# Performance work log

Hardware: AMD Instinct MI355X
Metric: run time of the kernel (lower is better)

Reference implementation:

```python
import jax, jax.numpy as jnp
import numpy as np

# ---- config constants (cfg) ----
AA, LP, Tc = 1.0, 1.0, 1.0
OMEGA_PHI, ALPHA_PHI, Lc = 1.0, 0.01, 1.0
CSE, CLE = 0.5, 0.00574
AC_PRE_SCALE = 1.0
AC1 = 2 * AA * LP * Tc
AC2 = LP * OMEGA_PHI * Tc
AC3 = LP * ALPHA_PHI * Tc / Lc**2

N, HID, NLAYERS, EMB = 65536, 128, 4, 64  # 2*EMB == HID


def setup_inputs() -> dict:
    key = jax.random.key(0)
    ks = jax.random.split(key, 6)
    x = jax.random.uniform(ks[0], (N, 2), dtype=jnp.float32)
    t = jax.random.uniform(ks[1], (N, 1), dtype=jnp.float32)
    B = jax.random.normal(ks[2], (3, EMB), dtype=jnp.float32)  # fourier features
    Wh = jax.random.normal(ks[3], (NLAYERS, HID, HID), dtype=jnp.float32) / np.sqrt(HID)
    bh = jnp.zeros((NLAYERS, HID), dtype=jnp.float32)
    Wout = jax.random.normal(ks[4], (HID, 2), dtype=jnp.float32) / np.sqrt(HID)
    bout = jnp.zeros((2,), dtype=jnp.float32)
    return {"x": x, "t": t, "B": B, "Wh": Wh, "bh": bh, "Wout": Wout, "bout": bout}


def reference(x, t, B, Wh, bh, Wout, bout):
    mirror = jnp.array([-1.0, 1.0], dtype=x.dtype)

    def mlp(xx, tt):  # xx:(2,), tt:(1,) -> (2,)
        z = jnp.concatenate([xx, tt])              # (3,)
        f = 2 * jnp.pi * (z @ B)                   # (EMB,)
        h = jnp.concatenate([jnp.sin(f), jnp.cos(f)])  # (HID,)
        def layer(h, wb):
            W, b = wb
            return jnp.tanh(h @ W + b), None
        h, _ = jax.lax.scan(layer, h, (Wh, bh))
        return h @ Wout + bout

    def net_u(xx, tt):  # hard-constrained (phi, c), symmetrized in x
        def hard_cons(xx_):
            phi, cl = jnp.tanh(mlp(xx_, tt)) / 2 + 0.5
            cl = cl * (1 - CSE + CLE)
            c = (CSE - CLE) * (-2 * phi**3 + 3 * phi**2) + cl
            return jnp.stack([phi, c])
        return (hard_cons(xx) + hard_cons(xx * mirror)) / 2

    def net_ac_point(xx, tt):  # Allen-Cahn residual at one collocation point
        phi, c = net_u(xx, tt)
        h_phi = -2 * phi**3 + 3 * phi**2
        dh_dphi = -6 * phi**2 + 6 * phi
        dg_dphi = 4 * phi**3 - 6 * phi**2 + 2 * phi
        dphi_dt = jax.jacrev(lambda t_: net_u(xx, t_)[0])(tt)          # (1,)
        hess = jax.hessian(lambda x_: net_u(x_, tt)[0])(xx)            # (2,2)
        nabla2phi = jnp.trace(hess)
        ac = (dphi_dt.squeeze()
              - AC1 * (c - h_phi * (CSE - CLE) - CLE) * (CSE - CLE) * dh_dphi
              + AC2 * dg_dphi
              - AC3 * nabla2phi)
        return ac / AC_PRE_SCALE

    return jax.vmap(net_ac_point)(x, t)  # (N,) PDE residuals
```

## Files before the change

kernel.cpp:

```cpp
#include <hip/hip_runtime.h>
#include <math.h>

#define NPTS_PER_WAVE 6

typedef _Float16 h8 __attribute__((ext_vector_type(8)));
typedef _Float16 h2 __attribute__((ext_vector_type(2)));
typedef __fp16   fp16x2 __attribute__((ext_vector_type(2)));
typedef float    f4 __attribute__((ext_vector_type(4)));
typedef unsigned int uint32;

#define CSE_C 0.5f
#define CLE_C 0.00574f
#define DCOEF (CSE_C - CLE_C)
#define KCOEF (1.0f - CSE_C + CLE_C)

__device__ __forceinline__ float tanh_fast(float xx) {
    float e = __expf(2.0f * xx);
    float r = __builtin_amdgcn_rcpf(e + 1.0f);
    return fmaf(-2.0f, r, 1.0f);
}
__device__ __forceinline__ unsigned short f2h(float a) {
    union { _Float16 h; unsigned short u; } ua; ua.h = (_Float16)a; return ua.u;
}
__device__ __forceinline__ h2 pkrtz(float a, float b) {
    union { fp16x2 f; h2 h; } x; x.f = __builtin_amdgcn_cvt_pkrtz(a, b); return x.h;
}
__device__ __forceinline__ uint32 pk2h(float a, float b) {
    union { h2 h; uint32 u; } x; x.h = pkrtz(a, b); return x.u;
}
__device__ __forceinline__ h8 h8_from4(uint32 a, uint32 b, uint32 c, uint32 d) {
    union { uint32 u[4]; h8 v; } x; x.u[0] = a; x.u[1] = b; x.u[2] = c; x.u[3] = d;
    return x.v;
}

extern "C" __global__ __launch_bounds__(256)
void pinn_prep(const float* __restrict__ Wh, uint32* __restrict__ Wp)
{
    int gid  = blockIdx.x * 256 + threadIdx.x;
    int d    = gid & 3;
    int lane = (gid >> 2) & 63;
    int kt   = (gid >> 8) & 3;
    int jo   = (gid >> 10) & 7;
    int L    = gid >> 13;
    int j    = kt * 32 + (lane >> 4) * 8 + 2 * d;
    int jout = jo * 16 + (lane & 15);
    float w0 = Wh[(L * 128 + j) * 128 + jout];
    float w1 = Wh[(L * 128 + j + 1) * 128 + jout];
    Wp[gid] = pk2h(w0, w1);
}

extern "C" __global__ __launch_bounds__(64, 2)
void pinn_mfma(const float* __restrict__ x, const float* __restrict__ t,
               const float* __restrict__ B, const uint32* __restrict__ Wp,
               const float* __restrict__ bh, const float* __restrict__ Wout,
               const float* __restrict__ bout, float* __restrict__ out, int npts)
{
    __shared__ __align__(16) unsigned short H[64][136];

    const int lane = threadIdx.x;
    const int c    = lane & 15;
    const int g    = lane >> 4;
    const int base_pt = blockIdx.x * NPTS_PER_WAVE;

    unsigned short* Hb = &H[0][0];

    uint4 wt[2][4];
    {
        const uint4* W0 = (const uint4*)Wp;
        #pragma unroll
        for (int kt = 0; kt < 4; ++kt) wt[0][kt] = W0[kt * 64 + lane];
        #pragma unroll
        for (int kt = 0; kt < 4; ++kt) wt[1][kt] = W0[(4 + kt) * 64 + lane];
    }

    {
        const float TWO_PI = 6.28318530717958647692f;
        const float Br0 = B[lane], Br1 = B[64 + lane], Br2 = B[128 + lane];
        const float b0 = TWO_PI * Br0, b1 = TWO_PI * Br1, b2 = TWO_PI * Br2;
        const float bsq = fmaf(b0, b0, b1 * b1);
        #pragma unroll
        for (int pl = 0; pl < 6; ++pl) {
            int pt = base_pt + pl; if (pt > npts - 1) pt = npts - 1;
            const float2 xx = *(const float2*)&x[2 * pt];
            const float tt = t[pt];
            const float uc = fmaf(xx.y, Br1, tt * Br2);
            const float ux = xx.x * Br0;
            #pragma unroll
            for (int mir = 0; mir < 2; ++mir) {
                float u = mir ? (uc - ux) : (uc + ux);
                float r = u - floorf(u);
                float sf = __builtin_amdgcn_sinf(r);
                float cf = __builtin_amdgcn_cosf(r);
                const int b  = pl * 2 + mir;
                const int rs = (b / 3) * 16 + (b % 3) * 5;
                Hb[(rs + 0) * 136 + lane] = f2h(sf);
                Hb[(rs + 1) * 136 + lane] = f2h(cf * b2);
                Hb[(rs + 2) * 136 + lane] = f2h(cf * b0);
                Hb[(rs + 3) * 136 + lane] = f2h(cf * b1);
                Hb[(rs + 4) * 136 + lane] = f2h(-sf * bsq);
                Hb[(rs + 0) * 136 + 64 + lane] = f2h(cf);
                Hb[(rs + 1) * 136 + 64 + lane] = f2h(-sf * b2);
                Hb[(rs + 2) * 136 + 64 + lane] = f2h(-sf * b0);
                Hb[(rs + 3) * 136 + 64 + lane] = f2h(-sf * b1);
                Hb[(rs + 4) * 136 + 64 + lane] = f2h(-cf * bsq);
            }
        }
    }
    asm volatile("s_waitcnt lgkmcnt(0)" ::: "memory");

    for (int L = 0; L < 4; ++L) {
        h8 bf[4][4];
        #pragma unroll
        for (int ct = 0; ct < 4; ++ct)
            #pragma unroll
            for (int kt = 0; kt < 4; ++kt)
                bf[ct][kt] = *(const h8*)&Hb[(ct * 16 + c) * 136 + kt * 32 + g * 8];

        const uint4* WL = (const uint4*)Wp + (size_t)L * 2048;
        const uint4* WN = WL + 2048;

        #pragma unroll
        for (int jo = 0; jo < 8; ++jo) {
            const int cur = jo & 1;
            f4 a0 = {0.f, 0.f, 0.f, 0.f}, a1 = {0.f, 0.f, 0.f, 0.f};
            f4 a2 = {0.f, 0.f, 0.f, 0.f}, a3 = {0.f, 0.f, 0.f, 0.f};
            #pragma unroll
            for (int kt = 0; kt < 4; ++kt) {
                union { uint4 u; h8 v; } af;
                af.u = wt[cur][kt];
                a0 = __builtin_amdgcn_mfma_f32_16x16x32_f16(af.v, bf[0][kt], a0, 0, 0, 0);
                a1 = __builtin_amdgcn_mfma_f32_16x16x32_f16(af.v, bf[1][kt], a1, 0, 0, 0);
                a2 = __builtin_amdgcn_mfma_f32_16x16x32_f16(af.v, bf[2][kt], a2, 0, 0, 0);
                a3 = __builtin_amdgcn_mfma_f32_16x16x32_f16(af.v, bf[3][kt], a3, 0, 0, 0);
            }
            if (jo < 6) {
                #pragma unroll
                for (int kt = 0; kt < 4; ++kt)
                    wt[cur][kt] = WL[((jo + 2) * 4 + kt) * 64 + lane];
            } else if (L < 3) {
                #pragma unroll
                for (int kt = 0; kt < 4; ++kt)
                    wt[cur][kt] = WN[((jo - 6) * 4 + kt) * 64 + lane];
            }
            union { h2 h[2]; uint2 u; } w0, w1, w2, w3;
            w0.h[0] = pkrtz(a0[0], a0[1]); w0.h[1] = pkrtz(a0[2], a0[3]);
            w1.h[0] = pkrtz(a1[0], a1[1]); w1.h[1] = pkrtz(a1[2], a1[3]);
            w2.h[0] = pkrtz(a2[0], a2[1]); w2.h[1] = pkrtz(a2[2], a2[3]);
            w3.h[0] = pkrtz(a3[0], a3[1]); w3.h[1] = pkrtz(a3[2], a3[3]);
            *(uint2*)&Hb[(0  + c) * 136 + jo * 16 + g * 4] = w0.u;
            *(uint2*)&Hb[(16 + c) * 136 + jo * 16 + g * 4] = w1.u;
            *(uint2*)&Hb[(32 + c) * 136 + jo * 16 + g * 4] = w2.u;
            *(uint2*)&Hb[(48 + c) * 136 + jo * 16 + g * 4] = w3.u;
        }
        asm volatile("s_waitcnt lgkmcnt(0)" ::: "memory");

        {
            const int jb = 2 * lane;
            const float2 bj = *(const float2*)&bh[L * 128 + jb];
            const h2 bias2 = pkrtz(bj.x, bj.y);
            const h2 m2 = {(_Float16)(-2.0f), (_Float16)(-2.0f)};
            #pragma unroll
            for (int b = 0; b < 12; ++b) {
                const int rs = (b / 3) * 16 + (b % 3) * 5;
                h2 vp = *(const h2*)&Hb[(rs + 0) * 136 + jb];
                h2 tp = *(const h2*)&Hb[(rs + 1) * 136 + jb];
                h2 pp = *(const h2*)&Hb[(rs + 2) * 136 + jb];
                h2 qp = *(const h2*)&Hb[(rs + 3) * 136 + jb];
                h2 Lp = *(const h2*)&Hb[(rs + 4) * 136 + jb];
                vp = vp + bias2;
                float y0 = tanh_fast((float)vp[0]);
                float y1 = tanh_fast((float)vp[1]);
                h2 yp = pkrtz(y0, y1);
                h2 sp = pkrtz(fmaf(-y0, y0, 1.f), fmaf(-y1, y1, 1.f));
                h2 qq = __builtin_elementwise_fma(pp, pp, qp * qp);
                h2 Ln = sp * __builtin_elementwise_fma(yp * m2, qq, Lp);
                *(h2*)&Hb[(rs + 0) * 136 + jb] = yp;
                *(h2*)&Hb[(rs + 1) * 136 + jb] = sp * tp;
                *(h2*)&Hb[(rs + 2) * 136 + jb] = sp * pp;
                *(h2*)&Hb[(rs + 3) * 136 + jb] = sp * qp;
                *(h2*)&Hb[(rs + 4) * 136 + jb] = Ln;
            }
        }
        asm volatile("s_waitcnt lgkmcnt(0)" ::: "memory");
    }

    {
        h8 afo[4];
        const int   mc  = c & 1;
        const float sel = (c < 2) ? 1.0f : 0.0f;
        #pragma unroll
        for (int kt = 0; kt < 4; ++kt) {
            uint32 u[4];
            #pragma unroll
            for (int d = 0; d < 4; ++d) {
                int k = kt * 32 + g * 8 + 2 * d;
                float w0 = Wout[k * 2 + mc] * sel;
                float w1 = Wout[(k + 1) * 2 + mc] * sel;
                u[d] = pk2h(w0, w1);
            }
            afo[kt] = h8_from4(u[0], u[1], u[2], u[3]);
        }
        h8 bfo[4][4];
        #pragma unroll
        for (int ct = 0; ct < 4; ++ct)
            #pragma unroll
            for (int kt = 0; kt < 4; ++kt)
                bfo[ct][kt] = *(const h8*)&Hb[(ct * 16 + c) * 136 + kt * 32 + g * 8];

        f4 ac0 = {0.f,0.f,0.f,0.f}, ac1 = {0.f,0.f,0.f,0.f};
        f4 ac2 = {0.f,0.f,0.f,0.f}, ac3 = {0.f,0.f,0.f,0.f};
        #pragma unroll
        for (int kt = 0; kt < 4; ++kt) {
            ac0 = __builtin_amdgcn_mfma_f32_16x16x32_f16(afo[kt], bfo[0][kt], ac0, 0, 0, 0);
            ac1 = __builtin_amdgcn_mfma_f32_16x16x32_f16(afo[kt], bfo[1][kt], ac1, 0, 0, 0);
            ac2 = __builtin_amdgcn_mfma_f32_16x16x32_f16(afo[kt], bfo[2][kt], ac2, 0, 0, 0);
            ac3 = __builtin_amdgcn_mfma_f32_16x16x32_f16(afo[kt], bfo[3][kt], ac3, 0, 0, 0);
        }
        float* S = (float*)Hb;
        if (g == 0) {
            f4 p0 = {ac0[0], ac0[1], ac1[0], ac1[1]};
            f4 p1 = {ac2[0], ac2[1], ac3[0], ac3[1]};
            *(f4*)&S[c * 4]      = p0;
            *(f4*)&S[64 + c * 4] = p1;
        }
        asm volatile("s_waitcnt lgkmcnt(0)" ::: "memory");

        if (lane < 6) {
            int pt = base_pt + lane;
            if (pt < npts) {
                float bo0 = bout[0], bo1 = bout[1];
                float ph = 0.f, cv = 0.f, ptd = 0.f, lp = 0.f;
                #pragma unroll
                for (int br = 0; br < 2; ++br) {
                    int b    = 2 * lane + br;
                    int ct   = b / 3;
                    int cc   = (b % 3) * 5;
                    int base = (ct >> 1) * 64;
                    int half = 2 * (ct & 1);
                    float o0v = S[base + (cc + 0) * 4 + half] + bo0;
                    float o0t = S[base + (cc + 1) * 4 + half];
                    float o0p = S[base + (cc + 2) * 4 + half];
                    float o0q = S[base + (cc + 3) * 4 + half];
                    float o0L = S[base + (cc + 4) * 4 + half];
                    float o1v = S[base + (cc + 0) * 4 + half + 1] + bo1;
                    float T = tanh_fast(o0v);
                    float p = fmaf(0.5f, T, 0.5f);
                    float s = 0.5f * fmaf(-T, T, 1.f);
                    float lap = s * o0L - 2.f * T * s * fmaf(o0p, o0p, o0q * o0q);
                    float cl = KCOEF * fmaf(0.5f, tanh_fast(o1v), 0.5f);
                    float cb = fmaf(DCOEF, (-2.f * p + 3.f) * p * p, cl);
                    ph  += 0.5f * p;
                    cv  += 0.5f * cb;
                    ptd += 0.5f * s * o0t;
                    lp  += 0.5f * lap;
                }
                float hph = (-2.f * ph + 3.f) * ph * ph;
                float dh  = 6.f * ph * (1.f - ph);
                float dg  = ((4.f * ph - 6.f) * ph + 2.f) * ph;
                float ac  = ptd
                          - 2.f * ((cv - hph * DCOEF - CLE_C) * DCOEF) * dh
                          + dg
                          - 0.01f * lp;
                out[pt] = ac;
            }
        }
    }
}

extern "C" void kernel_launch(void* const* d_in, const int* in_sizes, int n_in,
                              void* d_out, int out_size, void* d_ws, size_t ws_size,
                              hipStream_t stream) {
    const float* x    = (const float*)d_in[0];
    const float* t    = (const float*)d_in[1];
    const float* B    = (const float*)d_in[2];
    const float* Wh   = (const float*)d_in[3];
    const float* bh   = (const float*)d_in[4];
    const float* Wout = (const float*)d_in[5];
    const float* bout = (const float*)d_in[6];
    float* out = (float*)d_out;
    uint32* Wp = (uint32*)d_ws;

    const int npts = in_sizes[0] / 2;
    hipLaunchKernelGGL(pinn_prep, dim3(128), dim3(256), 0, stream, Wh, Wp);
    const int nb = (npts + NPTS_PER_WAVE - 1) / NPTS_PER_WAVE;
    hipLaunchKernelGGL(pinn_mfma, dim3(nb), dim3(64), 0, stream,
                       x, t, B, Wp, bh, Wout, bout, out, npts);
}
```

Before: 127.6 us.

## Switch hidden-layer GEMMs from 16x16x32 to 32x32x16 MFMA tiles

Re-packs the hidden weights and the activation tile so each layer uses 32x32x16 f16 MFMAs over two 32-row halves, where it used four 16-row tiles of 16x16x32. The point-row layout changes to groups of 6 branches per 32-row half, with padding rows zeroed. Weight prefetch becomes a rolling 4-fragment register ring. The aim is fewer MFMA issues and fewer fragment reloads per layer, at the cost of larger accumulator register usage and more register pressure.

```diff
diff --git a/kernel.cpp b/kernel.cpp
--- a/kernel.cpp
+++ b/kernel.cpp
@@ -7,6 +7,7 @@
 typedef _Float16 h2 __attribute__((ext_vector_type(2)));
 typedef __fp16   fp16x2 __attribute__((ext_vector_type(2)));
 typedef float    f4 __attribute__((ext_vector_type(4)));
+typedef float    f32x16 __attribute__((ext_vector_type(16)));
 typedef unsigned int uint32;
 
 #define CSE_C 0.5f
@@ -39,13 +40,13 @@
     int gid  = blockIdx.x * 256 + threadIdx.x;
     int d    = gid & 3;
     int lane = (gid >> 2) & 63;
-    int kt   = (gid >> 8) & 3;
-    int jo   = (gid >> 10) & 7;
+    int ks   = (gid >> 8) & 7;
+    int jt   = (gid >> 11) & 3;
     int L    = gid >> 13;
-    int j    = kt * 32 + (lane >> 4) * 8 + 2 * d;
-    int jout = jo * 16 + (lane & 15);
-    float w0 = Wh[(L * 128 + j) * 128 + jout];
-    float w1 = Wh[(L * 128 + j + 1) * 128 + jout];
+    int k0   = ks * 16 + (lane >> 5) * 8 + 2 * d;
+    int m    = jt * 32 + (lane & 31);
+    float w0 = Wh[(L * 128 + k0) * 128 + m];
+    float w1 = Wh[(L * 128 + k0 + 1) * 128 + m];
     Wp[gid] = pk2h(w0, w1);
 }
 
@@ -58,19 +59,17 @@
     __shared__ __align__(16) unsigned short H[64][136];
 
     const int lane = threadIdx.x;
-    const int c    = lane & 15;
-    const int g    = lane >> 4;
+    const int m31  = lane & 31;
+    const int kg8  = (lane >> 5) * 8;
     const int base_pt = blockIdx.x * NPTS_PER_WAVE;
 
     unsigned short* Hb = &H[0][0];
 
-    uint4 wt[2][4];
+    uint4 wf[4];
     {
         const uint4* W0 = (const uint4*)Wp;
         #pragma unroll
-        for (int kt = 0; kt < 4; ++kt) wt[0][kt] = W0[kt * 64 + lane];
-        #pragma unroll
-        for (int kt = 0; kt < 4; ++kt) wt[1][kt] = W0[(4 + kt) * 64 + lane];
+        for (int p = 0; p < 4; ++p) wf[p] = W0[p * 64 + lane];
     }
 
     {
@@ -78,6 +77,10 @@
         const float Br0 = B[lane], Br1 = B[64 + lane], Br2 = B[128 + lane];
         const float b0 = TWO_PI * Br0, b1 = TWO_PI * Br1, b2 = TWO_PI * Br2;
         const float bsq = fmaf(b0, b0, b1 * b1);
+        Hb[30 * 136 + lane] = 0; Hb[30 * 136 + 64 + lane] = 0;
+        Hb[31 * 136 + lane] = 0; Hb[31 * 136 + 64 + lane] = 0;
+        Hb[62 * 136 + lane] = 0; Hb[62 * 136 + 64 + lane] = 0;
+        Hb[63 * 136 + lane] = 0; Hb[63 * 136 + 64 + lane] = 0;
         #pragma unroll
         for (int pl = 0; pl < 6; ++pl) {
             int pt = base_pt + pl; if (pt > npts - 1) pt = npts - 1;
@@ -92,7 +95,7 @@
                 float sf = __builtin_amdgcn_sinf(r);
                 float cf = __builtin_amdgcn_cosf(r);
                 const int b  = pl * 2 + mir;
-                const int rs = (b / 3) * 16 + (b % 3) * 5;
+                const int rs = (b / 6) * 32 + (b % 6) * 5;
                 Hb[(rs + 0) * 136 + lane] = f2h(sf);
                 Hb[(rs + 1) * 136 + lane] = f2h(cf * b2);
                 Hb[(rs + 2) * 136 + lane] = f2h(cf * b0);
@@ -109,48 +112,41 @@
     asm volatile("s_waitcnt lgkmcnt(0)" ::: "memory");
 
     for (int L = 0; L < 4; ++L) {
-        h8 bf[4][4];
-        #pragma unroll
-        for (int ct = 0; ct < 4; ++ct)
-            #pragma unroll
-            for (int kt = 0; kt < 4; ++kt)
-                bf[ct][kt] = *(const h8*)&Hb[(ct * 16 + c) * 136 + kt * 32 + g * 8];
+        h8 bf0[8], bf1[8];
+        #pragma unroll
+        for (int ks = 0; ks < 8; ++ks) {
+            bf0[ks] = *(const h8*)&Hb[m31 * 136 + ks * 16 + kg8];
+            bf1[ks] = *(const h8*)&Hb[(32 + m31) * 136 + ks * 16 + kg8];
+        }
 
         const uint4* WL = (const uint4*)Wp + (size_t)L * 2048;
         const uint4* WN = WL + 2048;
 
         #pragma unroll
-        for (int jo = 0; jo < 8; ++jo) {
-            const int cur = jo & 1;
-            f4 a0 = {0.f, 0.f, 0.f, 0.f}, a1 = {0.f, 0.f, 0.f, 0.f};
-            f4 a2 = {0.f, 0.f, 0.f, 0.f}, a3 = {0.f, 0.f, 0.f, 0.f};
-            #pragma unroll
-            for (int kt = 0; kt < 4; ++kt) {
+        for (int jt = 0; jt < 4; ++jt) {
+            f32x16 a0 = {0.f,0.f,0.f,0.f,0.f,0.f,0.f,0.f,0.f,0.f,0.f,0.f,0.f,0.f,0.f,0.f};
+            f32x16 a1 = {0.f,0.f,0.f,0.f,0.f,0.f,0.f,0.f,0.f,0.f,0.f,0.f,0.f,0.f,0.f,0.f};
+            #pragma unroll
+            for (int ks = 0; ks < 8; ++ks) {
+                const int fi = jt * 8 + ks;
                 union { uint4 u; h8 v; } af;
-                af.u = wt[cur][kt];
-                a0 = __builtin_amdgcn_mfma_f32_16x16x32_f16(af.v, bf[0][kt], a0, 0, 0, 0);
-                a1 = __builtin_amdgcn_mfma_f32_16x16x32_f16(af.v, bf[1][kt], a1, 0, 0, 0);
-                a2 = __builtin_amdgcn_mfma_f32_16x16x32_f16(af.v, bf[2][kt], a2, 0, 0, 0);
-                a3 = __builtin_amdgcn_mfma_f32_16x16x32_f16(af.v, bf[3][kt], a3, 0, 0, 0);
-            }
-            if (jo < 6) {
-                #pragma unroll
-                for (int kt = 0; kt < 4; ++kt)
-                    wt[cur][kt] = WL[((jo + 2) * 4 + kt) * 64 + lane];
-            } else if (L < 3) {
-                #pragma unroll
-                for (int kt = 0; kt < 4; ++kt)
-                    wt[cur][kt] = WN[((jo - 6) * 4 + kt) * 64 + lane];
-            }
-            union { h2 h[2]; uint2 u; } w0, w1, w2, w3;
-            w0.h[0] = pkrtz(a0[0], a0[1]); w0.h[1] = pkrtz(a0[2], a0[3]);
-            w1.h[0] = pkrtz(a1[0], a1[1]); w1.h[1] = pkrtz(a1[2], a1[3]);
-            w2.h[0] = pkrtz(a2[0], a2[1]); w2.h[1] = pkrtz(a2[2], a2[3]);
-            w3.h[0] = pkrtz(a3[0], a3[1]); w3.h[1] = pkrtz(a3[2], a3[3]);
-            *(uint2*)&Hb[(0  + c) * 136 + jo * 16 + g * 4] = w0.u;
-            *(uint2*)&Hb[(16 + c) * 136 + jo * 16 + g * 4] = w1.u;
-            *(uint2*)&Hb[(32 + c) * 136 + jo * 16 + g * 4] = w2.u;
-            *(uint2*)&Hb[(48 + c) * 136 + jo * 16 + g * 4] = w3.u;
+                af.u = wf[fi & 3];
+                if (fi < 28)      wf[fi & 3] = WL[(fi + 4) * 64 + lane];
+                else if (L < 3)   wf[fi & 3] = WN[(fi - 28) * 64 + lane];
+                a0 = __builtin_amdgcn_mfma_f32_32x32x16_f16(af.v, bf0[ks], a0, 0, 0, 0);
+                a1 = __builtin_amdgcn_mfma_f32_32x32x16_f16(af.v, bf1[ks], a1, 0, 0, 0);
+            }
+            #pragma unroll
+            for (int q = 0; q < 4; ++q) {
+                union { h2 h[2]; uint2 u; } w0, w1;
+                w0.h[0] = pkrtz(a0[4*q+0], a0[4*q+1]);
+                w0.h[1] = pkrtz(a0[4*q+2], a0[4*q+3]);
+                w1.h[0] = pkrtz(a1[4*q+0], a1[4*q+1]);
+                w1.h[1] = pkrtz(a1[4*q+2], a1[4*q+3]);
+                const int jof = jt * 32 + q * 8 + (lane >> 5) * 4;
+                *(uint2*)&Hb[m31 * 136 + jof]        = w0.u;
+                *(uint2*)&Hb[(32 + m31) * 136 + jof] = w1.u;
+            }
         }
         asm volatile("s_waitcnt lgkmcnt(0)" ::: "memory");
 
@@ -161,7 +157,7 @@
             const h2 m2 = {(_Float16)(-2.0f), (_Float16)(-2.0f)};
             #pragma unroll
             for (int b = 0; b < 12; ++b) {
-                const int rs = (b / 3) * 16 + (b % 3) * 5;
+                const int rs = (b / 6) * 32 + (b % 6) * 5;
                 h2 vp = *(const h2*)&Hb[(rs + 0) * 136 + jb];
                 h2 tp = *(const h2*)&Hb[(rs + 1) * 136 + jb];
                 h2 pp = *(const h2*)&Hb[(rs + 2) * 136 + jb];
@@ -185,43 +181,32 @@
     }
 
     {
-        h8 afo[4];
-        const int   mc  = c & 1;
-        const float sel = (c < 2) ? 1.0f : 0.0f;
-        #pragma unroll
-        for (int kt = 0; kt < 4; ++kt) {
+        h8 afo[8];
+        const float sel = (m31 < 2) ? 1.0f : 0.0f;
+        const int   mi  = m31 & 1;
+        #pragma unroll
+        for (int ks = 0; ks < 8; ++ks) {
             uint32 u[4];
             #pragma unroll
             for (int d = 0; d < 4; ++d) {
-                int k = kt * 32 + g * 8 + 2 * d;
-                float w0 = Wout[k * 2 + mc] * sel;
-                float w1 = Wout[(k + 1) * 2 + mc] * sel;
-                u[d] = pk2h(w0, w1);
-            }
-            afo[kt] = h8_from4(u[0], u[1], u[2], u[3]);
-        }
-        h8 bfo[4][4];
-        #pragma unroll
-        for (int ct = 0; ct < 4; ++ct)
-            #pragma unroll
-            for (int kt = 0; kt < 4; ++kt)
-                bfo[ct][kt] = *(const h8*)&Hb[(ct * 16 + c) * 136 + kt * 32 + g * 8];
-
-        f4 ac0 = {0.f,0.f,0.f,0.f}, ac1 = {0.f,0.f,0.f,0.f};
-        f4 ac2 = {0.f,0.f,0.f,0.f}, ac3 = {0.f,0.f,0.f,0.f};
-        #pragma unroll
-        for (int kt = 0; kt < 4; ++kt) {
-            ac0 = __builtin_amdgcn_mfma_f32_16x16x32_f16(afo[kt], bfo[0][kt], ac0, 0, 0, 0);
-            ac1 = __builtin_amdgcn_mfma_f32_16x16x32_f16(afo[kt], bfo[1][kt], ac1, 0, 0, 0);
-            ac2 = __builtin_amdgcn_mfma_f32_16x16x32_f16(afo[kt], bfo[2][kt], ac2, 0, 0, 0);
-            ac3 = __builtin_amdgcn_mfma_f32_16x16x32_f16(afo[kt], bfo[3][kt], ac3, 0, 0, 0);
+                const int k0 = ks * 16 + kg8 + 2 * d;
+                u[d] = pk2h(Wout[k0 * 2 + mi] * sel, Wout[(k0 + 1) * 2 + mi] * sel);
+            }
+            afo[ks] = h8_from4(u[0], u[1], u[2], u[3]);
+        }
+        f32x16 a0 = {0.f,0.f,0.f,0.f,0.f,0.f,0.f,0.f,0.f,0.f,0.f,0.f,0.f,0.f,0.f,0.f};
+        f32x16 a1 = {0.f,0.f,0.f,0.f,0.f,0.f,0.f,0.f,0.f,0.f,0.f,0.f,0.f,0.f,0.f,0.f};
+        #pragma unroll
+        for (int ks = 0; ks < 8; ++ks) {
+            h8 b0 = *(const h8*)&Hb[m31 * 136 + ks * 16 + kg8];
+            h8 b1 = *(const h8*)&Hb[(32 + m31) * 136 + ks * 16 + kg8];
+            a0 = __builtin_amdgcn_mfma_f32_32x32x16_f16(afo[ks], b0, a0, 0, 0, 0);
+            a1 = __builtin_amdgcn_mfma_f32_32x32x16_f16(afo[ks], b1, a1, 0, 0, 0);
         }
         float* S = (float*)Hb;
-        if (g == 0) {
-            f4 p0 = {ac0[0], ac0[1], ac1[0], ac1[1]};
-            f4 p1 = {ac2[0], ac2[1], ac3[0], ac3[1]};
-            *(f4*)&S[c * 4]      = p0;
-            *(f4*)&S[64 + c * 4] = p1;
+        if (lane < 32) {
+            f4 pack = {a0[0], a0[1], a1[0], a1[1]};
+            *(f4*)&S[lane * 4] = pack;
         }
         asm volatile("s_waitcnt lgkmcnt(0)" ::: "memory");
 
@@ -232,17 +217,15 @@
                 float ph = 0.f, cv = 0.f, ptd = 0.f, lp = 0.f;
                 #pragma unroll
                 for (int br = 0; br < 2; ++br) {
-                    int b    = 2 * lane + br;
-                    int ct   = b / 3;
-                    int cc   = (b % 3) * 5;
-                    int base = (ct >> 1) * 64;
-                    int half = 2 * (ct & 1);
-                    float o0v = S[base + (cc + 0) * 4 + half] + bo0;
-                    float o0t = S[base + (cc + 1) * 4 + half];
-                    float o0p = S[base + (cc + 2) * 4 + half];
-                    float o0q = S[base + (cc + 3) * 4 + half];
-                    float o0L = S[base + (cc + 4) * 4 + half];
-                    float o1v = S[base + (cc + 0) * 4 + half + 1] + bo1;
+                    int b  = 2 * lane + br;
+                    int ct = b / 6;
+                    int n5 = (b % 6) * 5;
+                    float o0v = S[(n5 + 0) * 4 + 2 * ct] + bo0;
+                    float o0t = S[(n5 + 1) * 4 + 2 * ct];
+                    float o0p = S[(n5 + 2) * 4 + 2 * ct];
+                    float o0q = S[(n5 + 3) * 4 + 2 * ct];
+                    float o0L = S[(n5 + 4) * 4 + 2 * ct];
+                    float o1v = S[(n5 + 0) * 4 + 2 * ct + 1] + bo1;
                     float T = tanh_fast(o0v);
                     float p = fmaf(0.5f, T, 0.5f);
                     float s = 0.5f * fmaf(-T, T, 1.f);
```

Result: slower. 142.6 us (+11.8%).

## Process nine points per wave to amortize weight loads across more MFMA columns

Applied to the files above, without the earlier changes.

Raises the number of collocation points handled by each 64-lane block from 6 to 9, widening the MFMA N-dimension from 4 to 6 column tiles per weight fragment. Each weight tile streamed from global memory now feeds more MFMAs, cutting weight traffic and per-block overhead per point. The LDS tile grows to 96 rows and the register footprint rises (6x4 h8 B-fragments and 6 accumulators). That may reduce occupancy under launch_bounds(64,2) or cause spills. The output-stage layout of S is also reorganised to match the extra tiles.

```diff
diff --git a/kernel.cpp b/kernel.cpp
--- a/kernel.cpp
+++ b/kernel.cpp
@@ -1,7 +1,7 @@
 #include <hip/hip_runtime.h>
 #include <math.h>
 
-#define NPTS_PER_WAVE 6
+#define NPTS_PER_WAVE 9
 
 typedef _Float16 h8 __attribute__((ext_vector_type(8)));
 typedef _Float16 h2 __attribute__((ext_vector_type(2)));
@@ -55,7 +55,7 @@
                const float* __restrict__ bh, const float* __restrict__ Wout,
                const float* __restrict__ bout, float* __restrict__ out, int npts)
 {
-    __shared__ __align__(16) unsigned short H[64][136];
+    __shared__ __align__(16) unsigned short H[96][136];
 
     const int lane = threadIdx.x;
     const int c    = lane & 15;
@@ -79,7 +79,7 @@
         const float b0 = TWO_PI * Br0, b1 = TWO_PI * Br1, b2 = TWO_PI * Br2;
         const float bsq = fmaf(b0, b0, b1 * b1);
         #pragma unroll
-        for (int pl = 0; pl < 6; ++pl) {
+        for (int pl = 0; pl < 9; ++pl) {
             int pt = base_pt + pl; if (pt > npts - 1) pt = npts - 1;
             const float2 xx = *(const float2*)&x[2 * pt];
             const float tt = t[pt];
@@ -109,9 +109,9 @@
     asm volatile("s_waitcnt lgkmcnt(0)" ::: "memory");
 
     for (int L = 0; L < 4; ++L) {
-        h8 bf[4][4];
-        #pragma unroll
-        for (int ct = 0; ct < 4; ++ct)
+        h8 bf[6][4];
+        #pragma unroll
+        for (int ct = 0; ct < 6; ++ct)
             #pragma unroll
             for (int kt = 0; kt < 4; ++kt)
                 bf[ct][kt] = *(const h8*)&Hb[(ct * 16 + c) * 136 + kt * 32 + g * 8];
@@ -122,8 +122,7 @@
         #pragma unroll
         for (int jo = 0; jo < 8; ++jo) {
             const int cur = jo & 1;
-            f4 a0 = {0.f, 0.f, 0.f, 0.f}, a1 = {0.f, 0.f, 0.f, 0.f};
-            f4 a2 = {0.f, 0.f, 0.f, 0.f}, a3 = {0.f, 0.f, 0.f, 0.f};
+            f4 a0 = {0.f,0.f,0.f,0.f}, a1 = a0, a2 = a0, a3 = a0, a4 = a0, a5 = a0;
             #pragma unroll
             for (int kt = 0; kt < 4; ++kt) {
                 union { uint4 u; h8 v; } af;
@@ -132,6 +131,8 @@
                 a1 = __builtin_amdgcn_mfma_f32_16x16x32_f16(af.v, bf[1][kt], a1, 0, 0, 0);
                 a2 = __builtin_amdgcn_mfma_f32_16x16x32_f16(af.v, bf[2][kt], a2, 0, 0, 0);
                 a3 = __builtin_amdgcn_mfma_f32_16x16x32_f16(af.v, bf[3][kt], a3, 0, 0, 0);
+                a4 = __builtin_amdgcn_mfma_f32_16x16x32_f16(af.v, bf[4][kt], a4, 0, 0, 0);
+                a5 = __builtin_amdgcn_mfma_f32_16x16x32_f16(af.v, bf[5][kt], a5, 0, 0, 0);
             }
             if (jo < 6) {
                 #pragma unroll
@@ -142,15 +143,22 @@
                 for (int kt = 0; kt < 4; ++kt)
                     wt[cur][kt] = WN[((jo - 6) * 4 + kt) * 64 + lane];
             }
-            union { h2 h[2]; uint2 u; } w0, w1, w2, w3;
-            w0.h[0] = pkrtz(a0[0], a0[1]); w0.h[1] = pkrtz(a0[2], a0[3]);
-            w1.h[0] = pkrtz(a1[0], a1[1]); w1.h[1] = pkrtz(a1[2], a1[3]);
-            w2.h[0] = pkrtz(a2[0], a2[1]); w2.h[1] = pkrtz(a2[2], a2[3]);
-            w3.h[0] = pkrtz(a3[0], a3[1]); w3.h[1] = pkrtz(a3[2], a3[3]);
-            *(uint2*)&Hb[(0  + c) * 136 + jo * 16 + g * 4] = w0.u;
-            *(uint2*)&Hb[(16 + c) * 136 + jo * 16 + g * 4] = w1.u;
-            *(uint2*)&Hb[(32 + c) * 136 + jo * 16 + g * 4] = w2.u;
-            *(uint2*)&Hb[(48 + c) * 136 + jo * 16 + g * 4] = w3.u;
+            {
+                union { h2 h[2]; uint2 u; } w;
+                const int jof = jo * 16 + g * 4;
+                w.h[0] = pkrtz(a0[0], a0[1]); w.h[1] = pkrtz(a0[2], a0[3]);
+                *(uint2*)&Hb[(0  + c) * 136 + jof] = w.u;
+                w.h[0] = pkrtz(a1[0], a1[1]); w.h[1] = pkrtz(a1[2], a1[3]);
+                *(uint2*)&Hb[(16 + c) * 136 + jof] = w.u;
+                w.h[0] = pkrtz(a2[0], a2[1]); w.h[1] = pkrtz(a2[2], a2[3]);
+                *(uint2*)&Hb[(32 + c) * 136 + jof] = w.u;
+                w.h[0] = pkrtz(a3[0], a3[1]); w.h[1] = pkrtz(a3[2], a3[3]);
+                *(uint2*)&Hb[(48 + c) * 136 + jof] = w.u;
+                w.h[0] = pkrtz(a4[0], a4[1]); w.h[1] = pkrtz(a4[2], a4[3]);
+                *(uint2*)&Hb[(64 + c) * 136 + jof] = w.u;
+                w.h[0] = pkrtz(a5[0], a5[1]); w.h[1] = pkrtz(a5[2], a5[3]);
+                *(uint2*)&Hb[(80 + c) * 136 + jof] = w.u;
+            }
         }
         asm volatile("s_waitcnt lgkmcnt(0)" ::: "memory");
 
@@ -160,7 +168,7 @@
             const h2 bias2 = pkrtz(bj.x, bj.y);
             const h2 m2 = {(_Float16)(-2.0f), (_Float16)(-2.0f)};
             #pragma unroll
-            for (int b = 0; b < 12; ++b) {
+            for (int b = 0; b < 18; ++b) {
                 const int rs = (b / 3) * 16 + (b % 3) * 5;
                 h2 vp = *(const h2*)&Hb[(rs + 0) * 136 + jb];
                 h2 tp = *(const h2*)&Hb[(rs + 1) * 136 + jb];
@@ -200,49 +208,44 @@
             }
             afo[kt] = h8_from4(u[0], u[1], u[2], u[3]);
         }
-        h8 bfo[4][4];
-        #pragma unroll
-        for (int ct = 0; ct < 4; ++ct)
-            #pragma unroll
-            for (int kt = 0; kt < 4; ++kt)
-                bfo[ct][kt] = *(const h8*)&Hb[(ct * 16 + c) * 136 + kt * 32 + g * 8];
-
-        f4 ac0 = {0.f,0.f,0.f,0.f}, ac1 = {0.f,0.f,0.f,0.f};
-        f4 ac2 = {0.f,0.f,0.f,0.f}, ac3 = {0.f,0.f,0.f,0.f};
+        f4 ac[6];
+        #pragma unroll
+        for (int ct = 0; ct < 6; ++ct) { ac[ct] = f4{0.f, 0.f, 0.f, 0.f}; }
         #pragma unroll
         for (int kt = 0; kt < 4; ++kt) {
-            ac0 = __builtin_amdgcn_mfma_f32_16x16x32_f16(afo[kt], bfo[0][kt], ac0, 0, 0, 0);
-            ac1 = __builtin_amdgcn_mfma_f32_16x16x32_f16(afo[kt], bfo[1][kt], ac1, 0, 0, 0);
-            ac2 = __builtin_amdgcn_mfma_f32_16x16x32_f16(afo[kt], bfo[2][kt], ac2, 0, 0, 0);
-            ac3 = __builtin_amdgcn_mfma_f32_16x16x32_f16(afo[kt], bfo[3][kt], ac3, 0, 0, 0);
+            #pragma unroll
+            for (int ct = 0; ct < 6; ++ct) {
+                h8 bfo = *(const h8*)&Hb[(ct * 16 + c) * 136 + kt * 32 + g * 8];
+                ac[ct] = __builtin_amdgcn_mfma_f32_16x16x32_f16(afo[kt], bfo, ac[ct], 0, 0, 0);
+            }
         }
         float* S = (float*)Hb;
         if (g == 0) {
-            f4 p0 = {ac0[0], ac0[1], ac1[0], ac1[1]};
-            f4 p1 = {ac2[0], ac2[1], ac3[0], ac3[1]};
-            *(f4*)&S[c * 4]      = p0;
-            *(f4*)&S[64 + c * 4] = p1;
+            #pragma unroll
+            for (int ct = 0; ct < 6; ++ct) {
+                float2 pk = {ac[ct][0], ac[ct][1]};
+                *(float2*)&S[(ct * 16 + c) * 2] = pk;
+            }
         }
         asm volatile("s_waitcnt lgkmcnt(0)" ::: "memory");
 
-        if (lane < 6) {
+        if (lane < 9) {
             int pt = base_pt + lane;
             if (pt < npts) {
                 float bo0 = bout[0], bo1 = bout[1];
                 float ph = 0.f, cv = 0.f, ptd = 0.f, lp = 0.f;
                 #pragma unroll
                 for (int br = 0; br < 2; ++br) {
-                    int b    = 2 * lane + br;
-                    int ct   = b / 3;
-                    int cc   = (b % 3) * 5;
-                    int base = (ct >> 1) * 64;
-                    int half = 2 * (ct & 1);
-                    float o0v = S[base + (cc + 0) * 4 + half] + bo0;
-                    float o0t = S[base + (cc + 1) * 4 + half];
-                    float o0p = S[base + (cc + 2) * 4 + half];
-                    float o0q = S[base + (cc + 3) * 4 + half];
-                    float o0L = S[base + (cc + 4) * 4 + half];
-                    float o1v = S[base + (cc + 0) * 4 + half + 1] + bo1;
+                    int b  = 2 * lane + br;
+                    int ct = b / 3;
+                    int cc = (b % 3) * 5;
+                    const float* Sc = &S[(ct * 16 + cc) * 2];
+                    float o0v = Sc[0] + bo0;
+                    float o1v = Sc[1] + bo1;
+                    float o0t = Sc[2];
+                    float o0p = Sc[4];
+                    float o0q = Sc[6];
+                    float o0L = Sc[8];
                     float T = tanh_fast(o0v);
                     float p = fmaf(0.5f, T, 0.5f);
                     float s = 0.5f * fmaf(-T, T, 1.f);
@@ -257,11 +260,11 @@
                 float hph = (-2.f * ph + 3.f) * ph * ph;
                 float dh  = 6.f * ph * (1.f - ph);
                 float dg  = ((4.f * ph - 6.f) * ph + 2.f) * ph;
-                float ac  = ptd
+                float ac2 = ptd
                           - 2.f * ((cv - hph * DCOEF - CLE_C) * DCOEF) * dh
                           + dg
                           - 0.01f * lp;
-                out[pt] = ac;
+                out[pt] = ac2;
             }
         }
     }
```

After: 133.3 us. 4.5% more time.
